# Kernel tuning notes

Hardware: AMD Instinct MI355X
Metric: run time of the kernel (lower is better)

The kernel has to match this reference:

```python
import jax, jax.numpy as jnp
import numpy as np

N = 100000
E = 1600000
HID = 128
EPS = 1e-8


def _linear_params(key, fan_in, fan_out, bias=True, gain=1.0):
    kw, kb = jax.random.split(key)
    bound = gain / np.sqrt(fan_in)
    W = jax.random.uniform(kw, (fan_in, fan_out), jnp.float32, -bound, bound)
    if bias:
        b = jax.random.uniform(kb, (fan_out,), jnp.float32, -bound, bound)
        return W, b
    return W


def setup_inputs() -> dict:
    key = jax.random.key(0)
    ks = jax.random.split(key, 12)
    h = jax.random.normal(ks[0], (N, HID), jnp.float32)
    coord = jax.random.normal(ks[1], (N, 3), jnp.float32)
    edge_index = jax.random.randint(ks[2], (2, E), 0, N, jnp.int64)
    # edge_mlp: Linear(2*HID+1 -> HID), SiLU, Linear(HID -> HID), SiLU
    We1, be1 = _linear_params(ks[3], 2 * HID + 1, HID)
    We2, be2 = _linear_params(ks[4], HID, HID)
    # node_mlp: Linear(2*HID -> HID), SiLU, Linear(HID -> HID)
    Wn1, bn1 = _linear_params(ks[5], 2 * HID, HID)
    Wn2, bn2 = _linear_params(ks[6], HID, HID)
    # coord_mlp: Linear(HID -> HID), SiLU, Linear(HID -> 1, no bias, xavier gain=0.001)
    Wc1, bc1 = _linear_params(ks[7], HID, HID)
    Wc2 = _linear_params(ks[8], HID, 1, bias=False, gain=0.001 * np.sqrt(6.0 * HID / (HID + 1)))
    return {
        "h": h, "edge_index": edge_index, "coord": coord,
        "We1": We1, "be1": be1, "We2": We2, "be2": be2,
        "Wn1": Wn1, "bn1": bn1, "Wn2": Wn2, "bn2": bn2,
        "Wc1": Wc1, "bc1": bc1, "Wc2": Wc2,
    }


def _egcl(h, edge_index, coord, We1, be1, We2, be2, Wn1, bn1, Wn2, bn2, Wc1, bc1, Wc2):
    row, col = edge_index[0], edge_index[1]
    n = h.shape[0]
    # coord2radial (normalize=True, detach on norm)
    coord_diff = coord[row] - coord[col]                       # [E,3]
    radial = jnp.sum(coord_diff ** 2, axis=1, keepdims=True)   # [E,1]
    norm = jax.lax.stop_gradient(jnp.sqrt(radial)) + EPS
    coord_diff = coord_diff / norm
    # edge_model (no edge_attr, no attention)
    edge_in = jnp.concatenate([h[row], h[col], radial], axis=1)  # [E, 2H+1]
    m = jax.nn.silu(edge_in @ We1 + be1)
    m = jax.nn.silu(m @ We2 + be2)                               # [E,H]
    # coord_model (coords_agg='mean', tanh=False)
    phi_x = jax.nn.silu(m @ Wc1 + bc1) @ Wc2                     # [E,1]
    trans = coord_diff * phi_x                                   # [E,3]
    agg_c = jax.ops.segment_sum(trans, row, num_segments=n)
    cnt = jax.ops.segment_sum(jnp.ones((trans.shape[0],), trans.dtype), row, num_segments=n)
    agg_c = agg_c / jnp.clip(cnt, 1.0, None)[:, None]
    coord_out = coord + agg_c
    # node_model (residual=True)
    agg_h = jax.ops.segment_sum(m, row, num_segments=n)          # [N,H]
    node_in = jnp.concatenate([h, agg_h], axis=1)
    out = jax.nn.silu(node_in @ Wn1 + bn1) @ Wn2 + bn2
    h_out = h + out
    return h_out, coord_out


def reference(h, edge_index, coord, We1, be1, We2, be2, Wn1, bn1, Wn2, bn2, Wc1, bc1, Wc2):
    return _egcl(h, edge_index, coord, We1, be1, We2, be2, Wn1, bn1, Wn2, bn2, Wc1, bc1, Wc2)
```

## Files before the change

### kernel.cpp

```cpp
#include <hip/hip_runtime.h>

#define NN 100000
#define NE 1600000
#define HD 128
#define EPSV 1e-8f
#define EB 64
#define LPAD 136
#define CPAD 264

typedef unsigned short ushort_t;
typedef __attribute__((ext_vector_type(8))) short bf16x8;
typedef __attribute__((ext_vector_type(4))) float f32x4;

__device__ __forceinline__ float silu_f(float x) {
    return x * __builtin_amdgcn_rcpf(1.0f + __expf(-x));
}
__device__ __forceinline__ float b2f(unsigned short u) {
    union { unsigned int i; float f; } v; v.i = ((unsigned int)u) << 16; return v.f;
}
__device__ __forceinline__ unsigned short f2b(float f) {
    union { float f; unsigned int i; } v; v.f = f;
    unsigned int r = v.i + 0x7fff + ((v.i >> 16) & 1);
    return (unsigned short)(r >> 16);
}
__device__ __forceinline__ unsigned int cvt_pk_bf16(float lo, float hi) {
    unsigned int r;
    asm("v_cvt_pk_bf16_f32 %0, %1, %2" : "=v"(r) : "v"(lo), "v"(hi));
    return r;
}

extern "C" __global__ __launch_bounds__(256)
void k_prep(const float* __restrict__ We2, const float* __restrict__ Wc1,
            const float* __restrict__ We1, const float* __restrict__ Wn1,
            const float* __restrict__ Wn2,
            ushort_t* __restrict__ We2T, ushort_t* __restrict__ Wc1T,
            ushort_t* __restrict__ WabT, ushort_t* __restrict__ Wn1T,
            ushort_t* __restrict__ Wn2T)
{
    int id = blockIdx.x * 256 + threadIdx.x;
    if (id < 16384) {
        int n = id >> 7, k = id & 127;
        We2T[id] = f2b(We2[k * HD + n]);
    } else if (id < 32768) {
        int r = id - 16384; int n = r >> 7, k = r & 127;
        Wc1T[r] = f2b(Wc1[k * HD + n]);
    } else if (id < 65536) {
        int r = id - 32768; int j = r >> 7, k = r & 127;
        float v = (j < 128) ? We1[k * HD + j] : We1[(size_t)(128 + k) * HD + (j - 128)];
        WabT[r] = f2b(v);
    } else if (id < 98304) {
        int r = id - 65536; int j = r >> 8, k = r & 255;
        Wn1T[r] = f2b(Wn1[(size_t)k * HD + j]);
    } else if (id < 114688) {
        int r = id - 98304; int j = r >> 7, k = r & 127;
        Wn2T[r] = f2b(Wn2[k * HD + j]);
    }
}

extern "C" __global__ __launch_bounds__(256)
void k_hist(const int* __restrict__ ei, int* __restrict__ deg)
{
    int e = blockIdx.x * 256 + threadIdx.x;
    atomicAdd(&deg[ei[e]], 1);
}

extern "C" __global__ __launch_bounds__(1024)
void k_scan1(const int* __restrict__ deg, int* __restrict__ bsum)
{
    __shared__ int wsum[16];
    const int tid = threadIdx.x;
    const int lane = tid & 63, w = tid >> 6;
    int i = blockIdx.x * 1024 + tid;
    int v = (i < NN) ? deg[i] : 0;
#pragma unroll
    for (int off = 32; off > 0; off >>= 1) v += __shfl_xor(v, off, 64);
    if (lane == 0) wsum[w] = v;
    __syncthreads();
    if (tid == 0) {
        int s = 0;
#pragma unroll
        for (int k = 0; k < 16; k++) s += wsum[k];
        bsum[blockIdx.x] = s;
    }
}

extern "C" __global__ __launch_bounds__(128)
void k_scan2(const int* __restrict__ bsum, int* __restrict__ boff, int nb)
{
    __shared__ int wsum2[2];
    const int tid = threadIdx.x;
    const int lane = tid & 63, w = tid >> 6;
    int v = (tid < nb) ? bsum[tid] : 0;
    int s = v;
#pragma unroll
    for (int off = 1; off < 64; off <<= 1) {
        int t = __shfl_up(s, off, 64);
        if (lane >= off) s += t;
    }
    if (lane == 63) wsum2[w] = s;
    __syncthreads();
    int excl = ((w == 1) ? wsum2[0] : 0) + s - v;
    if (tid < nb) boff[tid] = excl;
}

extern "C" __global__ __launch_bounds__(1024)
void k_scan3(const int* __restrict__ deg, const int* __restrict__ boff,
             int* __restrict__ cursor)
{
    __shared__ int wsum[16];
    const int tid = threadIdx.x;
    const int lane = tid & 63, w = tid >> 6;
    int i = blockIdx.x * 1024 + tid;
    int v = (i < NN) ? deg[i] : 0;
    int s = v;
#pragma unroll
    for (int off = 1; off < 64; off <<= 1) {
        int t = __shfl_up(s, off, 64);
        if (lane >= off) s += t;
    }
    if (lane == 63) wsum[w] = s;
    __syncthreads();
    if (w == 0) {
        int ws = (lane < 16) ? wsum[lane] : 0;
#pragma unroll
        for (int off = 1; off < 16; off <<= 1) {
            int t = __shfl_up(ws, off, 64);
            if (lane >= off) ws += t;
        }
        if (lane < 16) wsum[lane] = ws;
    }
    __syncthreads();
    int excl = boff[blockIdx.x] + ((w > 0) ? wsum[w - 1] : 0) + s - v;
    if (i < NN) cursor[i] = excl;
}

extern "C" __global__ __launch_bounds__(256)
void k_sortids(const int* __restrict__ ei, int* __restrict__ cursor,
               int2* __restrict__ rc)
{
    int e = blockIdx.x * 256 + threadIdx.x;
    int r = ei[e], c = ei[NE + e];
    int slot = atomicAdd(&cursor[r], 1);
    rc[slot] = make_int2(r, c);
}

extern "C" __global__ __launch_bounds__(256)
void k_ab(const float* __restrict__ h, const ushort_t* __restrict__ WabT,
          const float* __restrict__ be1,
          ushort_t* __restrict__ A, ushort_t* __restrict__ B)
{
    __shared__ ushort_t hs[64][LPAD] __attribute__((aligned(16)));
    const int tid = threadIdx.x;
    const int n0 = blockIdx.x * 64;
    {
        int r = tid >> 2, seg = tid & 3;
        int n = n0 + r; if (n >= NN) n = n0;
        const float4* src = (const float4*)(h + (size_t)n * HD + seg * 32);
        uint2* dst = (uint2*)&hs[r][seg * 32];
#pragma unroll
        for (int i = 0; i < 8; i++) {
            float4 v = src[i];
            uint2 p; p.x = cvt_pk_bf16(v.x, v.y); p.y = cvt_pk_bf16(v.z, v.w);
            dst[i] = p;
        }
    }
    __syncthreads();
    const int wave = tid >> 6, lane = tid & 63;
    const int lr = lane & 15, lg = lane >> 4;
    f32x4 acc[16];
#pragma unroll
    for (int nt = 0; nt < 16; nt++) acc[nt] = (f32x4){0.f, 0.f, 0.f, 0.f};
#pragma unroll
    for (int ks = 0; ks < 4; ks++) {
        bf16x8 hf8 = *(const bf16x8*)&hs[wave * 16 + lr][ks * 32 + lg * 8];
#pragma unroll
        for (int nt = 0; nt < 16; nt++) {
            bf16x8 wf = *(const bf16x8*)(WabT + (size_t)(nt * 16 + lr) * HD + ks * 32 + lg * 8);
            acc[nt] = __builtin_amdgcn_mfma_f32_16x16x32_bf16(wf, hf8, acc[nt], 0, 0, 0);
        }
    }
    const int node = n0 + wave * 16 + lr;
    if (node < NN) {
#pragma unroll
        for (int nt = 0; nt < 16; nt++) {
            float4 bias = (nt < 8) ? ((const float4*)be1)[nt * 4 + lg]
                                   : (float4){0.f, 0.f, 0.f, 0.f};
            uint2 pk;
            pk.x = cvt_pk_bf16(acc[nt][0] + bias.x, acc[nt][1] + bias.y);
            pk.y = cvt_pk_bf16(acc[nt][2] + bias.z, acc[nt][3] + bias.w);
            if (nt < 8)
                *(uint2*)(A + (size_t)node * HD + nt * 16 + lg * 4) = pk;
            else
                *(uint2*)(B + (size_t)node * HD + (nt - 8) * 16 + lg * 4) = pk;
        }
    }
}

extern "C" __global__ __launch_bounds__(128, 4)
void k_edge(const int2* __restrict__ rc, const float* __restrict__ coord,
            const ushort_t* __restrict__ A, const ushort_t* __restrict__ B,
            const float* __restrict__ WeL, const float* __restrict__ be2,
            const ushort_t* __restrict__ We2T,
            const ushort_t* __restrict__ Wc1T,
            const float* __restrict__ bc1, const float* __restrict__ Wc2,
            float* __restrict__ agg_h, float* __restrict__ agg_c)
{
    __shared__ ushort_t m_lds[EB][LPAD] __attribute__((aligned(16)));
    __shared__ float cd_lds[EB][3];
    __shared__ int rows_s[EB];
    __shared__ float bias_lds[384] __attribute__((aligned(16)));
    __shared__ float wel_lds[128] __attribute__((aligned(16)));

    const int tid = threadIdx.x;
    const int e  = tid >> 1;
    const int hf = tid & 1;
    const int wave = tid >> 6, lane = tid & 63;
    const int lr = lane & 15, lg = lane >> 4;

    {
        int i = tid;
        bias_lds[i]       = (i < 128) ? be2[i] : 0.f;
        bias_lds[128 + i] = bc1[i];
        if (i < 128) bias_lds[256 + i] = Wc2[i];
        wel_lds[i] = WeL[i];
    }
    int2 rce = rc[blockIdx.x * EB + e];
    const int row = rce.x, col = rce.y;

    float c0 = coord[(size_t)row * 3 + 0] - coord[(size_t)col * 3 + 0];
    float c1 = coord[(size_t)row * 3 + 1] - coord[(size_t)col * 3 + 1];
    float c2 = coord[(size_t)row * 3 + 2] - coord[(size_t)col * 3 + 2];
    float radial = c0 * c0 + c1 * c1 + c2 * c2;
    if (hf == 0) {
        rows_s[e] = row;
        float inv = __builtin_amdgcn_rcpf(sqrtf(radial) + EPSV);
        cd_lds[e][0] = c0 * inv; cd_lds[e][1] = c1 * inv; cd_lds[e][2] = c2 * inv;
    }
    __syncthreads();

    {
        const bf16x8* A8 = (const bf16x8*)(A + (size_t)row * HD + hf * 64);
        const bf16x8* B8 = (const bf16x8*)(B + (size_t)col * HD + hf * 64);
        const float4* WL4 = (const float4*)wel_lds + hf * 16;
#pragma unroll
        for (int i = 0; i < 8; i++) {
            bf16x8 av = A8[i], bv = B8[i];
            float4 w0 = WL4[2 * i], w1 = WL4[2 * i + 1];
            float v0 = silu_f(b2f((ushort_t)av[0]) + b2f((ushort_t)bv[0]) + radial * w0.x);
            float v1 = silu_f(b2f((ushort_t)av[1]) + b2f((ushort_t)bv[1]) + radial * w0.y);
            float v2 = silu_f(b2f((ushort_t)av[2]) + b2f((ushort_t)bv[2]) + radial * w0.z);
            float v3 = silu_f(b2f((ushort_t)av[3]) + b2f((ushort_t)bv[3]) + radial * w0.w);
            float v4 = silu_f(b2f((ushort_t)av[4]) + b2f((ushort_t)bv[4]) + radial * w1.x);
            float v5 = silu_f(b2f((ushort_t)av[5]) + b2f((ushort_t)bv[5]) + radial * w1.y);
            float v6 = silu_f(b2f((ushort_t)av[6]) + b2f((ushort_t)bv[6]) + radial * w1.z);
            float v7 = silu_f(b2f((ushort_t)av[7]) + b2f((ushort_t)bv[7]) + radial * w1.w);
            uint4 p;
            p.x = cvt_pk_bf16(v0, v1); p.y = cvt_pk_bf16(v2, v3);
            p.z = cvt_pk_bf16(v4, v5); p.w = cvt_pk_bf16(v6, v7);
            *(uint4*)&m_lds[e][hf * 64 + i * 8] = p;
        }
    }

    f32x4 acc[2][8];
#pragma unroll
    for (int mt = 0; mt < 2; mt++)
#pragma unroll
        for (int nt = 0; nt < 8; nt++) acc[mt][nt] = (f32x4){0.f, 0.f, 0.f, 0.f};
#pragma unroll
    for (int ks = 0; ks < 4; ks++) {
        bf16x8 mf0 = *(const bf16x8*)&m_lds[wave * 32 + lr][ks * 32 + lg * 8];
        bf16x8 mf1 = *(const bf16x8*)&m_lds[wave * 32 + 16 + lr][ks * 32 + lg * 8];
#pragma unroll
        for (int nt = 0; nt < 8; nt++) {
            bf16x8 wf = *(const bf16x8*)(We2T + (size_t)(nt * 16 + lr) * HD + ks * 32 + lg * 8);
            acc[0][nt] = __builtin_amdgcn_mfma_f32_16x16x32_bf16(wf, mf0, acc[0][nt], 0, 0, 0);
            acc[1][nt] = __builtin_amdgcn_mfma_f32_16x16x32_bf16(wf, mf1, acc[1][nt], 0, 0, 0);
        }
    }
#pragma unroll
    for (int nt = 0; nt < 8; nt++) {
        float4 be2v = *(const float4*)&bias_lds[nt * 16 + lg * 4];
#pragma unroll
        for (int mt = 0; mt < 2; mt++) {
            float v0 = silu_f(acc[mt][nt][0] + be2v.x);
            float v1 = silu_f(acc[mt][nt][1] + be2v.y);
            float v2 = silu_f(acc[mt][nt][2] + be2v.z);
            float v3 = silu_f(acc[mt][nt][3] + be2v.w);
            uint2 pk; pk.x = cvt_pk_bf16(v0, v1); pk.y = cvt_pk_bf16(v2, v3);
            *(uint2*)&m_lds[wave * 32 + mt * 16 + lr][nt * 16 + lg * 4] = pk;
        }
    }

#pragma unroll
    for (int mt = 0; mt < 2; mt++)
#pragma unroll
        for (int nt = 0; nt < 8; nt++) acc[mt][nt] = (f32x4){0.f, 0.f, 0.f, 0.f};
#pragma unroll
    for (int ks = 0; ks < 4; ks++) {
        bf16x8 mf0 = *(const bf16x8*)&m_lds[wave * 32 + lr][ks * 32 + lg * 8];
        bf16x8 mf1 = *(const bf16x8*)&m_lds[wave * 32 + 16 + lr][ks * 32 + lg * 8];
#pragma unroll
        for (int nt = 0; nt < 8; nt++) {
            bf16x8 wf = *(const bf16x8*)(Wc1T + (size_t)(nt * 16 + lr) * HD + ks * 32 + lg * 8);
            acc[0][nt] = __builtin_amdgcn_mfma_f32_16x16x32_bf16(wf, mf0, acc[0][nt], 0, 0, 0);
            acc[1][nt] = __builtin_amdgcn_mfma_f32_16x16x32_bf16(wf, mf1, acc[1][nt], 0, 0, 0);
        }
    }

    float ph0 = 0.f, ph1 = 0.f;
#pragma unroll
    for (int nt = 0; nt < 8; nt++) {
        float4 bc1v = *(const float4*)&bias_lds[128 + nt * 16 + lg * 4];
        float4 wc2v = *(const float4*)&bias_lds[256 + nt * 16 + lg * 4];
        ph0 += silu_f(acc[0][nt][0] + bc1v.x) * wc2v.x
             + silu_f(acc[0][nt][1] + bc1v.y) * wc2v.y
             + silu_f(acc[0][nt][2] + bc1v.z) * wc2v.z
             + silu_f(acc[0][nt][3] + bc1v.w) * wc2v.w;
        ph1 += silu_f(acc[1][nt][0] + bc1v.x) * wc2v.x
             + silu_f(acc[1][nt][1] + bc1v.y) * wc2v.y
             + silu_f(acc[1][nt][2] + bc1v.z) * wc2v.z
             + silu_f(acc[1][nt][3] + bc1v.w) * wc2v.w;
    }
    ph0 += __shfl_xor(ph0, 16, 64); ph0 += __shfl_xor(ph0, 32, 64);
    ph1 += __shfl_xor(ph1, 16, 64); ph1 += __shfl_xor(ph1, 32, 64);
    if (lg == 0) {
        int e0 = wave * 32 + lr, e1 = e0 + 16;
        cd_lds[e0][0] *= ph0; cd_lds[e0][1] *= ph0; cd_lds[e0][2] *= ph0;
        cd_lds[e1][0] *= ph1; cd_lds[e1][1] *= ph1; cd_lds[e1][2] *= ph1;
    }

    __syncthreads();

    {
        const int j = tid;
        float acc_r = 0.f;
        int cur = rows_s[0];
        for (int es = 0; es < EB; es++) {
            int r = rows_s[es];
            if (r != cur) {
                atomicAdd(&agg_h[(size_t)cur * HD + j], acc_r);
                acc_r = 0.f; cur = r;
            }
            acc_r += b2f(m_lds[es][j]);
        }
        atomicAdd(&agg_h[(size_t)cur * HD + j], acc_r);
    }
    if (wave == 0) {
        int c = lane >> 4, sub = lane & 15;
        if (c < 3) {
            const int es0 = sub * 4, es1 = es0 + 4;
            float acc_r = 0.f;
            int cur = rows_s[es0];
            for (int es = es0; es < es1; es++) {
                int r = rows_s[es];
                if (r != cur) {
                    atomicAdd(&agg_c[(size_t)cur * 3 + c], acc_r);
                    acc_r = 0.f; cur = r;
                }
                acc_r += cd_lds[es][c];
            }
            atomicAdd(&agg_c[(size_t)cur * 3 + c], acc_r);
        }
    }
}

extern "C" __global__ __launch_bounds__(256)
void k_node(const float* __restrict__ h, const ushort_t* __restrict__ Wn1T,
            const float* __restrict__ bn1, const ushort_t* __restrict__ Wn2T,
            const float* __restrict__ bn2, const float* __restrict__ coord,
            const int* __restrict__ deg,
            float* __restrict__ hout ,
            float* __restrict__ cout )
{
    __shared__ ushort_t cs[64][CPAD] __attribute__((aligned(16)));
    __shared__ ushort_t us[64][LPAD] __attribute__((aligned(16)));
    const int tid = threadIdx.x;
    const int n0 = blockIdx.x * 64;
    {
        int r = tid >> 2, seg = tid & 3;
        int n = n0 + r; if (n >= NN) n = n0;
        const float4* s0 = (const float4*)(h + (size_t)n * HD + seg * 32);
        const float4* s1 = (const float4*)(hout + (size_t)n * HD + seg * 32);
        uint2* d0 = (uint2*)&cs[r][seg * 32];
        uint2* d1 = (uint2*)&cs[r][128 + seg * 32];
#pragma unroll
        for (int i = 0; i < 8; i++) {
            float4 v = s0[i];
            uint2 p; p.x = cvt_pk_bf16(v.x, v.y); p.y = cvt_pk_bf16(v.z, v.w);
            d0[i] = p;
            float4 w = s1[i];
            uint2 q; q.x = cvt_pk_bf16(w.x, w.y); q.y = cvt_pk_bf16(w.z, w.w);
            d1[i] = q;
        }
    }
    __syncthreads();
    const int wave = tid >> 6, lane = tid & 63;
    const int lr = lane & 15, lg = lane >> 4;

    f32x4 acc[8];
#pragma unroll
    for (int nt = 0; nt < 8; nt++) acc[nt] = (f32x4){0.f, 0.f, 0.f, 0.f};
#pragma unroll
    for (int ks = 0; ks < 8; ks++) {
        bf16x8 cf = *(const bf16x8*)&cs[wave * 16 + lr][ks * 32 + lg * 8];
#pragma unroll
        for (int nt = 0; nt < 8; nt++) {
            bf16x8 wf = *(const bf16x8*)(Wn1T + (size_t)(nt * 16 + lr) * 256 + ks * 32 + lg * 8);
            acc[nt] = __builtin_amdgcn_mfma_f32_16x16x32_bf16(wf, cf, acc[nt], 0, 0, 0);
        }
    }
#pragma unroll
    for (int nt = 0; nt < 8; nt++) {
        float4 b1 = ((const float4*)bn1)[nt * 4 + lg];
        float v0 = silu_f(acc[nt][0] + b1.x);
        float v1 = silu_f(acc[nt][1] + b1.y);
        float v2 = silu_f(acc[nt][2] + b1.z);
        float v3 = silu_f(acc[nt][3] + b1.w);
        uint2 pk; pk.x = cvt_pk_bf16(v0, v1); pk.y = cvt_pk_bf16(v2, v3);
        *(uint2*)&us[wave * 16 + lr][nt * 16 + lg * 4] = pk;
    }

    f32x4 acc2[8];
#pragma unroll
    for (int nt = 0; nt < 8; nt++) acc2[nt] = (f32x4){0.f, 0.f, 0.f, 0.f};
#pragma unroll
    for (int ks = 0; ks < 4; ks++) {
        bf16x8 uf = *(const bf16x8*)&us[wave * 16 + lr][ks * 32 + lg * 8];
#pragma unroll
        for (int nt = 0; nt < 8; nt++) {
            bf16x8 wf = *(const bf16x8*)(Wn2T + (size_t)(nt * 16 + lr) * HD + ks * 32 + lg * 8);
            acc2[nt] = __builtin_amdgcn_mfma_f32_16x16x32_bf16(wf, uf, acc2[nt], 0, 0, 0);
        }
    }
    const int node = n0 + wave * 16 + lr;
    if (node < NN) {
#pragma unroll
        for (int nt = 0; nt < 8; nt++) {
            float4 b2 = ((const float4*)bn2)[nt * 4 + lg];
            size_t idx = (size_t)node * HD + nt * 16 + lg * 4;
            float4 hv = *(const float4*)(h + idx);
            float4 o;
            o.x = hv.x + acc2[nt][0] + b2.x;
            o.y = hv.y + acc2[nt][1] + b2.y;
            o.z = hv.z + acc2[nt][2] + b2.z;
            o.w = hv.w + acc2[nt][3] + b2.w;
            *(float4*)(hout + idx) = o;
        }
        if (lg == 0) {
            float invc = __builtin_amdgcn_rcpf(fmaxf((float)deg[node], 1.0f));
#pragma unroll
            for (int i = 0; i < 3; i++) {
                size_t idx = (size_t)node * 3 + i;
                cout[idx] = coord[idx] + cout[idx] * invc;
            }
        }
    }
}

extern "C" void kernel_launch(void* const* d_in, const int* in_sizes, int n_in,
                              void* d_out, int out_size, void* d_ws, size_t ws_size,
                              hipStream_t stream)
{
    const float* h     = (const float*)d_in[0];
    const int*   ei    = (const int*)d_in[1];
    const float* coord = (const float*)d_in[2];
    const float* We1   = (const float*)d_in[3];
    const float* be1   = (const float*)d_in[4];
    const float* We2   = (const float*)d_in[5];
    const float* be2   = (const float*)d_in[6];
    const float* Wn1   = (const float*)d_in[7];
    const float* bn1   = (const float*)d_in[8];
    const float* Wn2   = (const float*)d_in[9];
    const float* bn2   = (const float*)d_in[10];
    const float* Wc1   = (const float*)d_in[11];
    const float* bc1   = (const float*)d_in[12];
    const float* Wc2   = (const float*)d_in[13];

    float* out   = (float*)d_out;
    float* agg_h = out;
    float* agg_c = out + (size_t)NN * HD;

    ushort_t* A    = (ushort_t*)d_ws;
    ushort_t* B    = A + (size_t)NN * HD;
    ushort_t* We2T = B + (size_t)NN * HD;
    ushort_t* Wc1T = We2T + 16384;
    ushort_t* WabT = Wc1T + 16384;
    ushort_t* Wn1T = WabT + 32768;
    ushort_t* Wn2T = Wn1T + 32768;
    int* deg    = (int*)(Wn2T + 16384);
    int* cursor = deg + NN;
    int* bsum   = cursor + NN;
    int* boff   = bsum + 128;
    int2* rc    = (int2*)(boff + 128);
    const float* WeL = We1 + (size_t)2 * HD * HD;

    const int scan_nb = (NN + 1023) / 1024;

    hipMemsetAsync(d_out, 0, (size_t)out_size * sizeof(float), stream);
    hipMemsetAsync(deg, 0, (size_t)NN * sizeof(int), stream);

    k_prep<<<448, 256, 0, stream>>>(We2, Wc1, We1, Wn1, Wn2,
                                    We2T, Wc1T, WabT, Wn1T, Wn2T);
    k_hist<<<NE / 256, 256, 0, stream>>>(ei, deg);
    k_ab<<<(NN + 63) / 64, 256, 0, stream>>>(h, WabT, be1, A, B);
    k_scan1<<<scan_nb, 1024, 0, stream>>>(deg, bsum);
    k_scan2<<<1, 128, 0, stream>>>(bsum, boff, scan_nb);
    k_scan3<<<scan_nb, 1024, 0, stream>>>(deg, boff, cursor);
    k_sortids<<<NE / 256, 256, 0, stream>>>(ei, cursor, rc);
    k_edge<<<NE / EB, 128, 0, stream>>>(rc, coord, A, B, WeL, be2,
                                        We2T, Wc1T, bc1, Wc2, agg_h, agg_c);
    k_node<<<(NN + 63) / 64, 256, 0, stream>>>(h, Wn1T, bn1, Wn2T, bn2, coord,
                                               deg, agg_h, agg_c);
}
```

Baseline: 889.1 us.

## Use 256 threads per edge block with one 16-edge MFMA tile per wave

The edge kernel now runs 4 waves per 64-edge block instead of 2. Each wave handles one 16-row MFMA tile rather than two, and each thread gathers a quarter of a feature row instead of a half. The agg_h scatter is split into two 32-edge halves. This halves the accumulator registers and raises occupancy to hide gather latency, at the cost of more atomics at segment boundaries and less reuse of the weight fragments loaded from global memory.

After: 1.453 ms. 63.5% more time.

```diff
diff --git a/kernel.cpp b/kernel.cpp
--- a/kernel.cpp
+++ b/kernel.cpp
@@ -196,7 +196,7 @@
     }
 }
 
-extern "C" __global__ __launch_bounds__(128, 4)
+extern "C" __global__ __launch_bounds__(256, 8)
 void k_edge(const int2* __restrict__ rc, const float* __restrict__ coord,
             const ushort_t* __restrict__ A, const ushort_t* __restrict__ B,
             const float* __restrict__ WeL, const float* __restrict__ be2,
@@ -212,18 +212,14 @@
     __shared__ float wel_lds[128] __attribute__((aligned(16)));
 
     const int tid = threadIdx.x;
-    const int e  = tid >> 1;
-    const int hf = tid & 1;
+    const int e  = tid >> 2;
+    const int q  = tid & 3;
     const int wave = tid >> 6, lane = tid & 63;
     const int lr = lane & 15, lg = lane >> 4;
 
-    {
-        int i = tid;
-        bias_lds[i]       = (i < 128) ? be2[i] : 0.f;
-        bias_lds[128 + i] = bc1[i];
-        if (i < 128) bias_lds[256 + i] = Wc2[i];
-        wel_lds[i] = WeL[i];
-    }
+    if (tid < 128) { bias_lds[tid] = be2[tid]; bias_lds[256 + tid] = Wc2[tid]; }
+    else           { bias_lds[tid] = bc1[tid - 128]; wel_lds[tid - 128] = WeL[tid - 128]; }
+
     int2 rce = rc[blockIdx.x * EB + e];
     const int row = rce.x, col = rce.y;
 
@@ -231,7 +227,7 @@
     float c1 = coord[(size_t)row * 3 + 1] - coord[(size_t)col * 3 + 1];
     float c2 = coord[(size_t)row * 3 + 2] - coord[(size_t)col * 3 + 2];
     float radial = c0 * c0 + c1 * c1 + c2 * c2;
-    if (hf == 0) {
+    if (q == 0) {
         rows_s[e] = row;
         float inv = __builtin_amdgcn_rcpf(sqrtf(radial) + EPSV);
         cd_lds[e][0] = c0 * inv; cd_lds[e][1] = c1 * inv; cd_lds[e][2] = c2 * inv;
@@ -239,11 +235,11 @@
     __syncthreads();
 
     {
-        const bf16x8* A8 = (const bf16x8*)(A + (size_t)row * HD + hf * 64);
-        const bf16x8* B8 = (const bf16x8*)(B + (size_t)col * HD + hf * 64);
-        const float4* WL4 = (const float4*)wel_lds + hf * 16;
-#pragma unroll
-        for (int i = 0; i < 8; i++) {
+        const bf16x8* A8 = (const bf16x8*)(A + (size_t)row * HD + q * 32);
+        const bf16x8* B8 = (const bf16x8*)(B + (size_t)col * HD + q * 32);
+        const float4* WL4 = (const float4*)wel_lds + q * 8;
+#pragma unroll
+        for (int i = 0; i < 4; i++) {
             bf16x8 av = A8[i], bv = B8[i];
             float4 w0 = WL4[2 * i], w1 = WL4[2 * i + 1];
             float v0 = silu_f(b2f((ushort_t)av[0]) + b2f((ushort_t)bv[0]) + radial * w0.x);
@@ -257,85 +253,69 @@
             uint4 p;
             p.x = cvt_pk_bf16(v0, v1); p.y = cvt_pk_bf16(v2, v3);
             p.z = cvt_pk_bf16(v4, v5); p.w = cvt_pk_bf16(v6, v7);
-            *(uint4*)&m_lds[e][hf * 64 + i * 8] = p;
-        }
-    }
-
-    f32x4 acc[2][8];
-#pragma unroll
-    for (int mt = 0; mt < 2; mt++)
-#pragma unroll
-        for (int nt = 0; nt < 8; nt++) acc[mt][nt] = (f32x4){0.f, 0.f, 0.f, 0.f};
+            *(uint4*)&m_lds[e][q * 32 + i * 8] = p;
+        }
+    }
+
+    f32x4 acc[8];
+#pragma unroll
+    for (int nt = 0; nt < 8; nt++) acc[nt] = (f32x4){0.f, 0.f, 0.f, 0.f};
 #pragma unroll
     for (int ks = 0; ks < 4; ks++) {
-        bf16x8 mf0 = *(const bf16x8*)&m_lds[wave * 32 + lr][ks * 32 + lg * 8];
-        bf16x8 mf1 = *(const bf16x8*)&m_lds[wave * 32 + 16 + lr][ks * 32 + lg * 8];
+        bf16x8 mf = *(const bf16x8*)&m_lds[wave * 16 + lr][ks * 32 + lg * 8];
 #pragma unroll
         for (int nt = 0; nt < 8; nt++) {
             bf16x8 wf = *(const bf16x8*)(We2T + (size_t)(nt * 16 + lr) * HD + ks * 32 + lg * 8);
-            acc[0][nt] = __builtin_amdgcn_mfma_f32_16x16x32_bf16(wf, mf0, acc[0][nt], 0, 0, 0);
-            acc[1][nt] = __builtin_amdgcn_mfma_f32_16x16x32_bf16(wf, mf1, acc[1][nt], 0, 0, 0);
+            acc[nt] = __builtin_amdgcn_mfma_f32_16x16x32_bf16(wf, mf, acc[nt], 0, 0, 0);
         }
     }
 #pragma unroll
     for (int nt = 0; nt < 8; nt++) {
         float4 be2v = *(const float4*)&bias_lds[nt * 16 + lg * 4];
-#pragma unroll
-        for (int mt = 0; mt < 2; mt++) {
-            float v0 = silu_f(acc[mt][nt][0] + be2v.x);
-            float v1 = silu_f(acc[mt][nt][1] + be2v.y);
-            float v2 = silu_f(acc[mt][nt][2] + be2v.z);
-            float v3 = silu_f(acc[mt][nt][3] + be2v.w);
-            uint2 pk; pk.x = cvt_pk_bf16(v0, v1); pk.y = cvt_pk_bf16(v2, v3);
-            *(uint2*)&m_lds[wave * 32 + mt * 16 + lr][nt * 16 + lg * 4] = pk;
-        }
-    }
-
-#pragma unroll
-    for (int mt = 0; mt < 2; mt++)
-#pragma unroll
-        for (int nt = 0; nt < 8; nt++) acc[mt][nt] = (f32x4){0.f, 0.f, 0.f, 0.f};
+        float v0 = silu_f(acc[nt][0] + be2v.x);
+        float v1 = silu_f(acc[nt][1] + be2v.y);
+        float v2 = silu_f(acc[nt][2] + be2v.z);
+        float v3 = silu_f(acc[nt][3] + be2v.w);
+        uint2 pk; pk.x = cvt_pk_bf16(v0, v1); pk.y = cvt_pk_bf16(v2, v3);
+        *(uint2*)&m_lds[wave * 16 + lr][nt * 16 + lg * 4] = pk;
+    }
+
+#pragma unroll
+    for (int nt = 0; nt < 8; nt++) acc[nt] = (f32x4){0.f, 0.f, 0.f, 0.f};
 #pragma unroll
     for (int ks = 0; ks < 4; ks++) {
-        bf16x8 mf0 = *(const bf16x8*)&m_lds[wave * 32 + lr][ks * 32 + lg * 8];
-        bf16x8 mf1 = *(const bf16x8*)&m_lds[wave * 32 + 16 + lr][ks * 32 + lg * 8];
+        bf16x8 mf = *(const bf16x8*)&m_lds[wave * 16 + lr][ks * 32 + lg * 8];
 #pragma unroll
         for (int nt = 0; nt < 8; nt++) {
             bf16x8 wf = *(const bf16x8*)(Wc1T + (size_t)(nt * 16 + lr) * HD + ks * 32 + lg * 8);
-            acc[0][nt] = __builtin_amdgcn_mfma_f32_16x16x32_bf16(wf, mf0, acc[0][nt], 0, 0, 0);
-            acc[1][nt] = __builtin_amdgcn_mfma_f32_16x16x32_bf16(wf, mf1, acc[1][nt], 0, 0, 0);
-        }
-    }
-
-    float ph0 = 0.f, ph1 = 0.f;
+            acc[nt] = __builtin_amdgcn_mfma_f32_16x16x32_bf16(wf, mf, acc[nt], 0, 0, 0);
+        }
+    }
+
+    float ph0 = 0.f;
 #pragma unroll
     for (int nt = 0; nt < 8; nt++) {
         float4 bc1v = *(const float4*)&bias_lds[128 + nt * 16 + lg * 4];
         float4 wc2v = *(const float4*)&bias_lds[256 + nt * 16 + lg * 4];
-        ph0 += silu_f(acc[0][nt][0] + bc1v.x) * wc2v.x
-             + silu_f(acc[0][nt][1] + bc1v.y) * wc2v.y
-             + silu_f(acc[0][nt][2] + bc1v.z) * wc2v.z
-             + silu_f(acc[0][nt][3] + bc1v.w) * wc2v.w;
-        ph1 += silu_f(acc[1][nt][0] + bc1v.x) * wc2v.x
-             + silu_f(acc[1][nt][1] + bc1v.y) * wc2v.y
-             + silu_f(acc[1][nt][2] + bc1v.z) * wc2v.z
-             + silu_f(acc[1][nt][3] + bc1v.w) * wc2v.w;
+        ph0 += silu_f(acc[nt][0] + bc1v.x) * wc2v.x
+             + silu_f(acc[nt][1] + bc1v.y) * wc2v.y
+             + silu_f(acc[nt][2] + bc1v.z) * wc2v.z
+             + silu_f(acc[nt][3] + bc1v.w) * wc2v.w;
     }
     ph0 += __shfl_xor(ph0, 16, 64); ph0 += __shfl_xor(ph0, 32, 64);
-    ph1 += __shfl_xor(ph1, 16, 64); ph1 += __shfl_xor(ph1, 32, 64);
     if (lg == 0) {
-        int e0 = wave * 32 + lr, e1 = e0 + 16;
+        int e0 = wave * 16 + lr;
         cd_lds[e0][0] *= ph0; cd_lds[e0][1] *= ph0; cd_lds[e0][2] *= ph0;
-        cd_lds[e1][0] *= ph1; cd_lds[e1][1] *= ph1; cd_lds[e1][2] *= ph1;
     }
 
     __syncthreads();
 
     {
-        const int j = tid;
+        const int j = tid & 127, g = tid >> 7;
+        const int es0 = g * 32, es1 = es0 + 32;
         float acc_r = 0.f;
-        int cur = rows_s[0];
-        for (int es = 0; es < EB; es++) {
+        int cur = rows_s[es0];
+        for (int es = es0; es < es1; es++) {
             int r = rows_s[es];
             if (r != cur) {
                 atomicAdd(&agg_h[(size_t)cur * HD + j], acc_r);
@@ -507,7 +487,7 @@
     k_scan2<<<1, 128, 0, stream>>>(bsum, boff, scan_nb);
     k_scan3<<<scan_nb, 1024, 0, stream>>>(deg, boff, cursor);
     k_sortids<<<NE / 256, 256, 0, stream>>>(ei, cursor, rc);
-    k_edge<<<NE / EB, 128, 0, stream>>>(rc, coord, A, B, WeL, be2,
+    k_edge<<<NE / EB, 256, 0, stream>>>(rc, coord, A, B, WeL, be2,
                                         We2T, Wc1T, bc1, Wc2, agg_h, agg_c);
     k_node<<<(NN + 63) / 64, 256, 0, stream>>>(h, Wn1T, bn1, Wn2T, bn2, coord,
                                                deg, agg_h, agg_c);
```
